# Performance work log

Hardware: AMD Instinct MI355X
Metric: run time of the kernel (lower is better)

The kernel has to match this reference:

```python
import jax, jax.numpy as jnp
import numpy as np

B = 1024      # graphs
NODES = 128   # nodes per graph (uniform -> batch_ptr = arange(B+1)*NODES)
IN = 64
HID = 256
OUT = 128
NBLK = 3
TAU = 0.25


def _ln(x, g, b):
    # LayerNorm over last dim, eps=1e-5 (torch default)
    mu = jnp.mean(x, axis=-1, keepdims=True)
    var = jnp.mean((x - mu) ** 2, axis=-1, keepdims=True)
    return (x - mu) / jnp.sqrt(var + 1e-5) * g + b


def setup_inputs() -> dict:
    key = jax.random.key(0)
    ks = jax.random.split(key, 4)
    sc = 0.05
    return {
        "H": jax.random.normal(ks[0], (B * NODES, IN), jnp.float32),
        "batch_ptr": jnp.arange(B + 1, dtype=jnp.int32) * NODES,
        # ResNetMLP params: stem Linear(IN->HID)+LN, NBLK residual blocks
        # Linear(HID->HID)+LN+ReLU, head Linear(HID->OUT)+LN (last_norm=True).
        "W_in": jax.random.normal(ks[1], (IN, HID), jnp.float32) * sc,
        "b_in": jnp.zeros((HID,), jnp.float32),
        "g_in": jnp.ones((HID,), jnp.float32),
        "beta_in": jnp.zeros((HID,), jnp.float32),
        "Wb": jax.random.normal(ks[2], (NBLK, HID, HID), jnp.float32) * sc,
        "bb": jnp.zeros((NBLK, HID), jnp.float32),
        "gb": jnp.ones((NBLK, HID), jnp.float32),
        "betab": jnp.zeros((NBLK, HID), jnp.float32),
        "W_out": jax.random.normal(ks[3], (HID, OUT), jnp.float32) * sc,
        "b_out": jnp.zeros((OUT,), jnp.float32),
        "g_out": jnp.ones((OUT,), jnp.float32),
        "beta_out": jnp.zeros((OUT,), jnp.float32),
    }


def reference(H, batch_ptr, W_in, b_in, g_in, beta_in, Wb, bb, gb, betab,
              W_out, b_out, g_out, beta_out):
    # ResNetMLP projection (dropout is identity in eval)
    x = jax.nn.relu(_ln(H @ W_in + b_in, g_in, beta_in))          # [N, HID]
    for k in range(NBLK):
        x = x + jax.nn.relu(_ln(x @ Wb[k] + bb[k], gb[k], betab[k]))
    z = _ln(x @ W_out + b_out, g_out, beta_out)                   # [N, OUT]

    # Uniform-size graphs: ragged per-graph loop vectorizes to [Bg, n, OUT]
    Bg = batch_ptr.shape[0] - 1
    n = H.shape[0] // Bg
    z3 = z.reshape(Bg, n, OUT)

    # s_i = mean_j ||z_i - z_j||_2 (includes j=i, distance 0)
    sq = jnp.sum(z3 * z3, axis=-1)                                # [Bg, n]
    d2 = sq[:, :, None] + sq[:, None, :] - 2.0 * jnp.einsum("bid,bjd->bij", z3, z3)
    d = jnp.sqrt(jnp.maximum(d2, 0.0) + 1e-12)                    # [Bg, n, n]
    s = jnp.mean(d, axis=-1)                                      # [Bg, n]

    w = jax.nn.softmax(s / TAU, axis=-1)                          # [Bg, n]
    v_loc = jnp.einsum("bi,bid->bd", w, z3)                       # [Bg, OUT]
    return v_loc, w
```

## Files before the change

### kernel.cpp

```cpp
#include <hip/hip_runtime.h>
#include <stdint.h>


typedef __attribute__((ext_vector_type(8))) short bf16x8;
typedef __attribute__((ext_vector_type(4))) float f32x4;

#define XB_STRIDE 264
#define YB_STRIDE 260
#define ZB_STRIDE 136
#define LDS_PAR   66560
#define LDS_TOTAL 69632

__device__ __forceinline__ unsigned int rne16(float f) {
  unsigned int u = __builtin_bit_cast(unsigned int, f);
  return u + 0x7fffu + ((u >> 16) & 1u);
}
__device__ __forceinline__ unsigned short f2bf(float f) {
  return (unsigned short)(rne16(f) >> 16);
}
__device__ __forceinline__ float bf2f(unsigned short h) {
  unsigned int u = ((unsigned int)h) << 16;
  return __builtin_bit_cast(float, u);
}
__device__ __forceinline__ f32x4 zero4() {
  f32x4 v; v.x = 0.f; v.y = 0.f; v.z = 0.f; v.w = 0.f; return v;
}
template <int CTRL>
__device__ __forceinline__ float dpp_add(float v) {
  int p = __builtin_amdgcn_update_dpp(0, __builtin_bit_cast(int, v),
                                      CTRL, 0xF, 0xF, true);
  return v + __builtin_bit_cast(float, p);
}
__device__ __forceinline__ float red16(float v) {
  v = dpp_add<0xB1>(v);
  v = dpp_add<0x4E>(v);
  v = dpp_add<0x141>(v);
  v = dpp_add<0x140>(v);
  return v;
}

__global__ void prep_weights(const float* __restrict__ Win, const float* __restrict__ Wb,
                             const float* __restrict__ Wout, unsigned short* __restrict__ ws) {
  int g = blockIdx.x * 256 + threadIdx.x;
  if (g >= 30720) return;
  const float* W; int N; int local;
  if (g < 2048) { W = Win; N = 256; local = g; }
  else if (g < 26624) {
    int i = g - 2048; int blk = i >> 13; local = i & 8191;
    W = Wb + blk * 65536; N = 256;
  } else { W = Wout; N = 128; local = g - 26624; }
  int f = local >> 6, lane = local & 63;
  int NTL = N >> 4;
  int kc = f / NTL, ntile = f - kc * NTL;
  int n = ntile * 16 + (lane & 15);
  int k0 = kc * 32 + (lane >> 4) * 8;
  unsigned short o[8];
#pragma unroll
  for (int e = 0; e < 8; ++e) o[e] = f2bf(W[(size_t)(k0 + e) * N + n]);
  *reinterpret_cast<uint4*>(ws + (size_t)g * 8) = *reinterpret_cast<uint4*>(o);
}

template <int KL, int N, int MODE>
__device__ __forceinline__ void layer(unsigned short* __restrict__ Xb,
                                      float* __restrict__ Yb, float* __restrict__ par,
                                      const unsigned short* __restrict__ Wf,
                                      int tid, int wave, int lane,
                                      const float* __restrict__ bias,
                                      const float* __restrict__ gam,
                                      const float* __restrict__ bet,
                                      float (&xprev)[16],
                                      unsigned short* __restrict__ Z, size_t rowglob) {
  constexpr int NT = N / 128;
  constexpr int NTL = N / 16;
  constexpr int KC = KL / 32;
  constexpr int J = N / 64;
  const int wr = wave >> 3, wc = wave & 7;
  const int q = lane >> 4, l16 = lane & 15;
  const int rowbase = wr * 32;
  const int colbase = wc * 16 * NT;
  const unsigned short* Wl = Wf + lane * 8;

  f32x4 acc[2][NT];
#pragma unroll
  for (int mt = 0; mt < 2; ++mt)
#pragma unroll
    for (int nt = 0; nt < NT; ++nt) acc[mt][nt] = zero4();

  bf16x8 bcur[NT];
#pragma unroll
  for (int nt = 0; nt < NT; ++nt)
    bcur[nt] = *reinterpret_cast<const bf16x8*>(Wl + (size_t)(wc * NT + nt) * 512);

  __syncthreads();
  if (tid < 3 * N) {
    float v = (tid < N) ? bias[tid] : (tid < 2 * N) ? gam[tid - N] : bet[tid - 2 * N];
    par[tid] = v;
  }
#pragma unroll
  for (int kc = 0; kc < KC; ++kc) {
    bf16x8 bnext[NT];
    if (kc + 1 < KC) {
#pragma unroll
      for (int nt = 0; nt < NT; ++nt)
        bnext[nt] = *reinterpret_cast<const bf16x8*>(
            Wl + (size_t)((kc + 1) * NTL + wc * NT + nt) * 512);
    }
    const int kk = kc * 32 + q * 8;
    bf16x8 a0 = *reinterpret_cast<const bf16x8*>(Xb + (rowbase + l16) * XB_STRIDE + kk);
    bf16x8 a1 = *reinterpret_cast<const bf16x8*>(Xb + (rowbase + 16 + l16) * XB_STRIDE + kk);
#pragma unroll
    for (int nt = 0; nt < NT; ++nt)
      acc[0][nt] = __builtin_amdgcn_mfma_f32_16x16x32_bf16(a0, bcur[nt], acc[0][nt], 0, 0, 0);
#pragma unroll
    for (int nt = 0; nt < NT; ++nt)
      acc[1][nt] = __builtin_amdgcn_mfma_f32_16x16x32_bf16(a1, bcur[nt], acc[1][nt], 0, 0, 0);
    if (kc + 1 < KC) {
#pragma unroll
      for (int nt = 0; nt < NT; ++nt) bcur[nt] = bnext[nt];
    }
  }

  __syncthreads();

#pragma unroll
  for (int mt = 0; mt < 2; ++mt)
#pragma unroll
    for (int nt = 0; nt < NT; ++nt) {
      const int col = colbase + 16 * nt + l16;
#pragma unroll
      for (int r = 0; r < 4; ++r)
        Yb[(rowbase + 16 * mt + 4 * q + r) * YB_STRIDE + col] = acc[mt][nt][r];
    }
  __syncthreads();

  const int row = wave * 4 + q;
  const int cb = l16 * 4;
  float y[4 * J];
#pragma unroll
  for (int j = 0; j < J; ++j)
    *reinterpret_cast<f32x4*>(y + 4 * j) =
        *reinterpret_cast<const f32x4*>(Yb + row * YB_STRIDE + cb + 64 * j);
  float bv[4 * J], gv[4 * J], ev[4 * J];
#pragma unroll
  for (int j = 0; j < J; ++j) {
    *reinterpret_cast<f32x4*>(bv + 4 * j) = *reinterpret_cast<const f32x4*>(par + cb + 64 * j);
    *reinterpret_cast<f32x4*>(gv + 4 * j) = *reinterpret_cast<const f32x4*>(par + N + cb + 64 * j);
    *reinterpret_cast<f32x4*>(ev + 4 * j) = *reinterpret_cast<const f32x4*>(par + 2 * N + cb + 64 * j);
  }
  float s1 = 0.f, s2 = 0.f;
#pragma unroll
  for (int e = 0; e < 4 * J; ++e) {
    y[e] += bv[e];
    s1 += y[e]; s2 = __builtin_fmaf(y[e], y[e], s2);
  }
  s1 = red16(s1); s2 = red16(s2);
  const float mu = s1 * (1.0f / N);
  const float var = s2 * (1.0f / N) - mu * mu;
  const float rstd = rsqrtf(var + 1e-5f);
  const float nmr = -mu * rstd;
  unsigned int pkall[2 * J];
#pragma unroll
  for (int j = 0; j < J; ++j) {
#pragma unroll
    for (int i = 0; i < 4; ++i) {
      const int e = 4 * j + i;
      float t = __builtin_fmaf(y[e], rstd, nmr);
      float o = __builtin_fmaf(t, gv[e], ev[e]);
      float xv;
      if constexpr (MODE == 0) { xv = fmaxf(o, 0.f); xprev[e] = xv; }
      else if constexpr (MODE == 1) { xv = xprev[e] + fmaxf(o, 0.f); xprev[e] = xv; }
      else { xv = o; }
      if (i & 1)
        pkall[2 * j + (i >> 1)] = __builtin_amdgcn_perm(rne16(xv),
                       rne16(__builtin_bit_cast(float, pkall[2 * j + (i >> 1)])), 0x07060302);
      else
        pkall[2 * j + (i >> 1)] = __builtin_bit_cast(unsigned int, xv);
    }
  }
  if constexpr (MODE != 2) {
    __syncthreads();
    unsigned int* Xw = reinterpret_cast<unsigned int*>(Xb);
#pragma unroll
    for (int j = 0; j < J; ++j)
      *reinterpret_cast<uint2*>(Xw + row * 132 + 2 * l16 + 32 * j) =
          *reinterpret_cast<uint2*>(pkall + 2 * j);
  } else {
#pragma unroll
    for (int j = 0; j < J; ++j)
      *reinterpret_cast<uint2*>(Z + (rowglob + row) * 128 + cb + 64 * j) =
          *reinterpret_cast<uint2*>(pkall + 2 * j);
  }
}

__global__ __attribute__((amdgpu_flat_work_group_size(1024, 1024), amdgpu_waves_per_eu(4)))
void mlp_main(const float* __restrict__ H, const unsigned short* __restrict__ ws,
              const float* __restrict__ b_in, const float* __restrict__ g_in,
              const float* __restrict__ beta_in,
              const float* __restrict__ bb, const float* __restrict__ gb,
              const float* __restrict__ betab,
              const float* __restrict__ b_out, const float* __restrict__ g_out,
              const float* __restrict__ beta_out,
              unsigned short* __restrict__ Z) {
  extern __shared__ char smem[];
  unsigned short* Xb = (unsigned short*)smem;
  float* Yb = (float*)smem;
  float* par = (float*)(smem + LDS_PAR);
  const int tid = threadIdx.x;
  const int wave = tid >> 6, lane = tid & 63;
  const size_t rowglob = (size_t)blockIdx.x * 64;

  {
    int row = tid >> 4, c4 = (tid & 15) * 4;
    float4 f = *reinterpret_cast<const float4*>(H + (rowglob + row) * 64 + c4);
    uint2 o;
    o.x = __builtin_amdgcn_perm(rne16(f.y), rne16(f.x), 0x07060302);
    o.y = __builtin_amdgcn_perm(rne16(f.w), rne16(f.z), 0x07060302);
    *reinterpret_cast<uint2*>(Xb + row * XB_STRIDE + c4) = o;
  }

  float xprev[16];
  layer<64, 256, 0>(Xb, Yb, par, ws,           tid, wave, lane, b_in,     g_in,     beta_in,  xprev, Z, rowglob);
  layer<256, 256, 1>(Xb, Yb, par, ws + 16384,  tid, wave, lane, bb,       gb,       betab,    xprev, Z, rowglob);
  layer<256, 256, 1>(Xb, Yb, par, ws + 81920,  tid, wave, lane, bb + 256, gb + 256, betab + 256, xprev, Z, rowglob);
  layer<256, 256, 1>(Xb, Yb, par, ws + 147456, tid, wave, lane, bb + 512, gb + 512, betab + 512, xprev, Z, rowglob);
  layer<256, 128, 2>(Xb, Yb, par, ws + 212992, tid, wave, lane, b_out,    g_out,    beta_out, xprev, Z, rowglob);
}

__global__ __attribute__((amdgpu_flat_work_group_size(512, 512)))
void pool_main(const unsigned short* __restrict__ Z, float* __restrict__ out) {
  __shared__ unsigned short Zb[128 * ZB_STRIDE];
  __shared__ float sqv[128], sm[128], smw[128];
  const int tid = threadIdx.x;
  const int g = blockIdx.x;
  const int wave = tid >> 6, lane = tid & 63;
  const int q = lane >> 4, l16 = lane & 15;

  {
    int zr = tid >> 2, zc = (tid & 3) * 32;
    const uint4* zp = reinterpret_cast<const uint4*>(Z + ((size_t)g * 128 + zr) * 128 + zc);
    uint4* zd = reinterpret_cast<uint4*>(Zb + zr * ZB_STRIDE + zc);
    zd[0] = zp[0]; zd[1] = zp[1]; zd[2] = zp[2]; zd[3] = zp[3];
  }
  __syncthreads();

  f32x4 g2[8];
#pragma unroll
  for (int nt = 0; nt < 8; ++nt) g2[nt] = zero4();
#pragma unroll
  for (int ks = 0; ks < 4; ++ks) {
    int kk = ks * 32 + q * 8;
    bf16x8 a = *reinterpret_cast<const bf16x8*>(Zb + (16 * wave + l16) * ZB_STRIDE + kk);
#pragma unroll
    for (int nt = 0; nt < 8; ++nt) {
      bf16x8 bfr = *reinterpret_cast<const bf16x8*>(Zb + (16 * nt + l16) * ZB_STRIDE + kk);
      g2[nt] = __builtin_amdgcn_mfma_f32_16x16x32_bf16(a, bfr, g2[nt], 0, 0, 0);
    }
  }
  if ((l16 >> 2) == q) {
#pragma unroll
    for (int nt = 0; nt < 8; ++nt)
      if (nt == wave) {
#pragma unroll
        for (int r = 0; r < 4; ++r)
          if ((l16 & 3) == r) sqv[16 * wave + l16] = g2[nt][r];
      }
  }
  __syncthreads();
  float sqi[4];
#pragma unroll
  for (int r = 0; r < 4; ++r) sqi[r] = sqv[16 * wave + q * 4 + r];
  float sp[4] = {0.f, 0.f, 0.f, 0.f};
#pragma unroll
  for (int nt = 0; nt < 8; ++nt) {
    float sqj = sqv[16 * nt + l16];
#pragma unroll
    for (int r = 0; r < 4; ++r) {
      float d2 = sqi[r] + sqj - 2.0f * g2[nt][r];
      sp[r] += sqrtf(fmaxf(d2, 0.f) + 1e-12f);
    }
  }
#pragma unroll
  for (int d = 1; d < 16; d <<= 1) {
#pragma unroll
    for (int r = 0; r < 4; ++r) { float t = sp[r]; t += __shfl_xor(t, d); sp[r] = t; }
  }
  if (l16 == 0) {
#pragma unroll
    for (int r = 0; r < 4; ++r) sm[16 * wave + q * 4 + r] = sp[r] * (1.0f / 128.0f);
  }
  __syncthreads();
  if (wave == 0) {
    float l0 = sm[lane] * 4.0f;
    float l1 = sm[lane + 64] * 4.0f;
    float mx = fmaxf(l0, l1);
#pragma unroll
    for (int d = 1; d < 64; d <<= 1) mx = fmaxf(mx, __shfl_xor(mx, d));
    float e0 = __expf(l0 - mx), e1 = __expf(l1 - mx);
    float ss = e0 + e1;
#pragma unroll
    for (int d = 1; d < 64; d <<= 1) ss += __shfl_xor(ss, d);
    float inv = 1.0f / ss;
    float w0 = e0 * inv, w1 = e1 * inv;
    smw[lane] = w0;
    smw[lane + 64] = w1;
    out[131072 + g * 128 + lane] = w0;
    out[131072 + g * 128 + 64 + lane] = w1;
  }
  __syncthreads();
  {
    int c = 16 * wave + l16;
    float acv = 0.f;
#pragma unroll
    for (int i0 = 0; i0 < 32; ++i0) {
      int i = q * 32 + i0;
      acv += smw[i] * bf2f(Zb[i * ZB_STRIDE + c]);
    }
    acv += __shfl_xor(acv, 16);
    acv += __shfl_xor(acv, 32);
    if (q == 0) out[g * 128 + c] = acv;
  }
}

extern "C" void kernel_launch(void* const* d_in, const int* in_sizes, int n_in,
                              void* d_out, int out_size, void* d_ws, size_t ws_size,
                              hipStream_t stream) {
  (void)in_sizes; (void)n_in; (void)out_size; (void)ws_size;
  const float* H        = (const float*)d_in[0];
  const float* W_in     = (const float*)d_in[2];
  const float* b_in     = (const float*)d_in[3];
  const float* g_in     = (const float*)d_in[4];
  const float* beta_in  = (const float*)d_in[5];
  const float* Wb       = (const float*)d_in[6];
  const float* bb       = (const float*)d_in[7];
  const float* gb       = (const float*)d_in[8];
  const float* betab    = (const float*)d_in[9];
  const float* W_out    = (const float*)d_in[10];
  const float* b_out    = (const float*)d_in[11];
  const float* g_out    = (const float*)d_in[12];
  const float* beta_out = (const float*)d_in[13];
  float* out = (float*)d_out;
  unsigned short* ws = (unsigned short*)d_ws;
  unsigned short* Z = ws + 262144;

  prep_weights<<<120, 256, 0, stream>>>(W_in, Wb, W_out, ws);
  hipFuncSetAttribute(reinterpret_cast<const void*>(mlp_main),
                      hipFuncAttributeMaxDynamicSharedMemorySize, LDS_TOTAL);
  mlp_main<<<2048, 1024, LDS_TOTAL, stream>>>(H, ws, b_in, g_in, beta_in,
                                              bb, gb, betab, b_out, g_out, beta_out, Z);
  pool_main<<<1024, 512, 0, stream>>>(Z, out);
}
```

Baseline: 241.3 us.

## Shrink MLP blocks to 32 rows and 512 threads with halved LDS

The fused MLP kernel now runs 512-thread blocks, each covering 32 rows instead of 64. All 8 waves split only the output columns, and the 2x4 wave split over rows and columns is removed. LDS per block is halved, and the per-layer bias, gamma and beta loads are moved into the loops that use them to cut register pressure. The goal is more resident blocks per CU and better latency hiding. The cost is that each block reloads the full weight matrices for half as many rows, doubling global and L2 weight traffic.

```diff
diff --git a/kernel.cpp b/kernel.cpp
--- a/kernel.cpp
+++ b/kernel.cpp
@@ -8,8 +8,8 @@
 #define XB_STRIDE 264
 #define YB_STRIDE 260
 #define ZB_STRIDE 136
-#define LDS_PAR   66560
-#define LDS_TOTAL 69632
+#define LDS_PAR   33280
+#define LDS_TOTAL 36352
 
 __device__ __forceinline__ unsigned int rne16(float f) {
   unsigned int u = __builtin_bit_cast(unsigned int, f);
@@ -74,9 +74,8 @@
   constexpr int NTL = N / 16;
   constexpr int KC = KL / 32;
   constexpr int J = N / 64;
-  const int wr = wave >> 3, wc = wave & 7;
+  const int wc = wave;
   const int q = lane >> 4, l16 = lane & 15;
-  const int rowbase = wr * 32;
   const int colbase = wc * 16 * NT;
   const unsigned short* Wl = Wf + lane * 8;
 
@@ -92,9 +91,9 @@
     bcur[nt] = *reinterpret_cast<const bf16x8*>(Wl + (size_t)(wc * NT + nt) * 512);
 
   __syncthreads();
-  if (tid < 3 * N) {
-    float v = (tid < N) ? bias[tid] : (tid < 2 * N) ? gam[tid - N] : bet[tid - 2 * N];
-    par[tid] = v;
+  for (int t = tid; t < 3 * N; t += 512) {
+    float v = (t < N) ? bias[t] : (t < 2 * N) ? gam[t - N] : bet[t - 2 * N];
+    par[t] = v;
   }
 #pragma unroll
   for (int kc = 0; kc < KC; ++kc) {
@@ -106,8 +105,8 @@
             Wl + (size_t)((kc + 1) * NTL + wc * NT + nt) * 512);
     }
     const int kk = kc * 32 + q * 8;
-    bf16x8 a0 = *reinterpret_cast<const bf16x8*>(Xb + (rowbase + l16) * XB_STRIDE + kk);
-    bf16x8 a1 = *reinterpret_cast<const bf16x8*>(Xb + (rowbase + 16 + l16) * XB_STRIDE + kk);
+    bf16x8 a0 = *reinterpret_cast<const bf16x8*>(Xb + (l16) * XB_STRIDE + kk);
+    bf16x8 a1 = *reinterpret_cast<const bf16x8*>(Xb + (16 + l16) * XB_STRIDE + kk);
 #pragma unroll
     for (int nt = 0; nt < NT; ++nt)
       acc[0][nt] = __builtin_amdgcn_mfma_f32_16x16x32_bf16(a0, bcur[nt], acc[0][nt], 0, 0, 0);
@@ -129,29 +128,25 @@
       const int col = colbase + 16 * nt + l16;
 #pragma unroll
       for (int r = 0; r < 4; ++r)
-        Yb[(rowbase + 16 * mt + 4 * q + r) * YB_STRIDE + col] = acc[mt][nt][r];
+        Yb[(16 * mt + 4 * q + r) * YB_STRIDE + col] = acc[mt][nt][r];
     }
   __syncthreads();
 
   const int row = wave * 4 + q;
   const int cb = l16 * 4;
   float y[4 * J];
-#pragma unroll
-  for (int j = 0; j < J; ++j)
+  float s1 = 0.f, s2 = 0.f;
+#pragma unroll
+  for (int j = 0; j < J; ++j) {
     *reinterpret_cast<f32x4*>(y + 4 * j) =
         *reinterpret_cast<const f32x4*>(Yb + row * YB_STRIDE + cb + 64 * j);
-  float bv[4 * J], gv[4 * J], ev[4 * J];
-#pragma unroll
-  for (int j = 0; j < J; ++j) {
-    *reinterpret_cast<f32x4*>(bv + 4 * j) = *reinterpret_cast<const f32x4*>(par + cb + 64 * j);
-    *reinterpret_cast<f32x4*>(gv + 4 * j) = *reinterpret_cast<const f32x4*>(par + N + cb + 64 * j);
-    *reinterpret_cast<f32x4*>(ev + 4 * j) = *reinterpret_cast<const f32x4*>(par + 2 * N + cb + 64 * j);
-  }
-  float s1 = 0.f, s2 = 0.f;
-#pragma unroll
-  for (int e = 0; e < 4 * J; ++e) {
-    y[e] += bv[e];
-    s1 += y[e]; s2 = __builtin_fmaf(y[e], y[e], s2);
+    f32x4 bv = *reinterpret_cast<const f32x4*>(par + cb + 64 * j);
+#pragma unroll
+    for (int i = 0; i < 4; ++i) {
+      const int e = 4 * j + i;
+      y[e] += bv[i];
+      s1 += y[e]; s2 = __builtin_fmaf(y[e], y[e], s2);
+    }
   }
   s1 = red16(s1); s2 = red16(s2);
   const float mu = s1 * (1.0f / N);
@@ -161,11 +156,13 @@
   unsigned int pkall[2 * J];
 #pragma unroll
   for (int j = 0; j < J; ++j) {
+    f32x4 gv = *reinterpret_cast<const f32x4*>(par + N + cb + 64 * j);
+    f32x4 ev = *reinterpret_cast<const f32x4*>(par + 2 * N + cb + 64 * j);
 #pragma unroll
     for (int i = 0; i < 4; ++i) {
       const int e = 4 * j + i;
       float t = __builtin_fmaf(y[e], rstd, nmr);
-      float o = __builtin_fmaf(t, gv[e], ev[e]);
+      float o = __builtin_fmaf(t, gv[i], ev[i]);
       float xv;
       if constexpr (MODE == 0) { xv = fmaxf(o, 0.f); xprev[e] = xv; }
       else if constexpr (MODE == 1) { xv = xprev[e] + fmaxf(o, 0.f); xprev[e] = xv; }
@@ -192,7 +189,7 @@
   }
 }
 
-__global__ __attribute__((amdgpu_flat_work_group_size(1024, 1024), amdgpu_waves_per_eu(4)))
+__global__ __attribute__((amdgpu_flat_work_group_size(512, 512), amdgpu_waves_per_eu(4)))
 void mlp_main(const float* __restrict__ H, const unsigned short* __restrict__ ws,
               const float* __restrict__ b_in, const float* __restrict__ g_in,
               const float* __restrict__ beta_in,
@@ -207,7 +204,7 @@
   float* par = (float*)(smem + LDS_PAR);
   const int tid = threadIdx.x;
   const int wave = tid >> 6, lane = tid & 63;
-  const size_t rowglob = (size_t)blockIdx.x * 64;
+  const size_t rowglob = (size_t)blockIdx.x * 32;
 
   {
     int row = tid >> 4, c4 = (tid & 15) * 4;
@@ -345,7 +342,7 @@
   prep_weights<<<120, 256, 0, stream>>>(W_in, Wb, W_out, ws);
   hipFuncSetAttribute(reinterpret_cast<const void*>(mlp_main),
                       hipFuncAttributeMaxDynamicSharedMemorySize, LDS_TOTAL);
-  mlp_main<<<2048, 1024, LDS_TOTAL, stream>>>(H, ws, b_in, g_in, beta_in,
-                                              bb, gb, betab, b_out, g_out, beta_out, Z);
+  mlp_main<<<4096, 512, LDS_TOTAL, stream>>>(H, ws, b_in, g_in, beta_in,
+                                             bb, gb, betab, b_out, g_out, beta_out, Z);
   pool_main<<<1024, 512, 0, stream>>>(Z, out);
 }
```

Result: faster. 227.4 us (-5.8%).
